# Kernel tuning notes

Hardware: AMD Instinct MI355X
Metric: run time of the kernel (lower is better)

The kernel has to match this reference:

```python
import jax, jax.numpy as jnp
import numpy as np

D_MODEL = 1024
NUM_HEADS = 16
HEAD_DIM = D_MODEL // NUM_HEADS          # 64
ROT_W = HEAD_DIM // 2                    # partial_factor=(0.0, 0.5) -> rotary on first half
MAX_LEN = 2048
BASE = 10000.0


def _rope_tables(max_len):
    # theta over even dims of ROT_W, each repeated twice (interleaved pairs): [t0,t0,t1,t1,...]
    theta = 1.0 / (BASE ** (np.arange(0, ROT_W, 2, dtype=np.float32) / ROT_W))  # [ROT_W/2]
    m = np.arange(max_len, dtype=np.float32)[:, None] * theta[None, :]          # [max_len, ROT_W/2]
    m = np.repeat(m, 2, axis=-1)                                                # [max_len, ROT_W]
    return jnp.asarray(np.cos(m)), jnp.asarray(np.sin(m))


def _rotate(x):
    # interleaved pairs (x0, x1) -> (-x1, x0)
    xr = x.reshape(x.shape[:-1] + (-1, 2))
    rot = jnp.stack([-xr[..., 1], xr[..., 0]], axis=-1)
    return rot.reshape(x.shape)


def setup_inputs() -> dict:
    key = jax.random.key(0)
    k1, k2, k3, k4 = jax.random.split(key, 4)
    B, L, H, E = 2, 2048, NUM_HEADS, HEAD_DIM
    return {
        "queries": jax.random.normal(k1, (B, L, H, E), jnp.float32),
        "keys": jax.random.normal(k2, (B, L, H, E), jnp.float32),
        "values": jax.random.normal(k3, (B, L, H, E), jnp.float32),
        "bias_weight": jax.random.normal(k4, (2, H), jnp.float32) * 0.02,  # BinaryAttentionBias embedding
        "n_vars": 32,
        "n_tokens": 64,
    }


def reference(queries, keys, values, bias_weight, n_vars, n_tokens):
    B, L, H, E = queries.shape
    q = queries.transpose(0, 2, 1, 3)  # [B,H,L,E]
    k = keys.transpose(0, 2, 1, 3)     # [B,H,L,E]

    # --- partial rotary projection (shared for q and k), seq_id = arange(L) ---
    cos, sin = _rope_tables(MAX_LEN)
    seq = jnp.arange(n_vars * n_tokens)
    c = cos[seq][None, None]  # [1,1,L,ROT_W]
    s = sin[seq][None, None]

    def rope(x):
        xr = x[..., :ROT_W]
        return jnp.concatenate([c * xr + s * _rotate(xr), x[..., ROT_W:]], axis=-1)

    q = rope(q)
    k = rope(k)

    scale = 1.0 / np.sqrt(E).astype(np.float32)

    # --- binary attention bias: per-head scalar by variable-id equality ---
    var_id = jnp.repeat(jnp.arange(n_vars), n_tokens)          # [L]
    same_var = var_id[:, None] == var_id[None, :]              # [L,L]
    bias = jnp.where(same_var[None, :, :],
                     bias_weight[1][:, None, None],
                     bias_weight[0][:, None, None])            # [H,L,L]

    # --- TimerMultivariateMask: causal in time, full across variables ---
    time_id = seq % n_tokens
    causal_bad = time_id[None, :] > time_id[:, None]           # key time > query time
    attn_mask = jnp.where(causal_bad[None], -jnp.inf, bias)    # [H,L,L]

    scores = jnp.einsum('bhle,bhse->bhls', q, k)               # [B,H,L,L]
    A = jax.nn.softmax(scale * scores + attn_mask[None], axis=-1)
    V = jnp.einsum('bhls,bshd->blhd', A, values)               # [B,L,H,E]
    return V
```

## Files before the change

kernel.cpp:

```cpp
#include <hip/hip_runtime.h>

typedef unsigned short u16;
typedef unsigned int u32;

typedef __attribute__((ext_vector_type(8))) __bf16 bf16x8;
typedef __attribute__((ext_vector_type(4))) float floatx4;

#define B_ 2
#define L_ 2048
#define H_ 16
#define E_ 64
#define QK_ELEMS (B_ * H_ * L_ * E_)
#define WS_OFF 128

static __device__ __forceinline__ float bf2f(u16 v) {
  u32 u = ((u32)v) << 16;
  return __builtin_bit_cast(float, u);
}
static __device__ __forceinline__ u16 f2bf(float x) {
  u32 u = __builtin_bit_cast(u32, x);
  u32 r = (u + 0x7FFFu + ((u >> 16) & 1u)) >> 16;
  return (u16)r;
}

static __device__ __forceinline__ u32 cvtpk_bf16(float lo, float hi) {
  u32 r;
  asm("v_cvt_pk_bf16_f32 %0, %1, %2" : "=v"(r) : "v"(lo), "v"(hi));
  return r;
}

static __device__ __forceinline__ float exp2_fast(float x) {
  float r;
  asm("v_exp_f32 %0, %1" : "=v"(r) : "v"(x));
  return r;
}

static __device__ __forceinline__ void sincos_fast(float a, float* s, float* c) {
  const float INV2PI = 0.15915494309189535f;
  float r = a * INV2PI;
  r = r - floorf(r);
  float ss, cc;
  asm("v_sin_f32 %0, %1" : "=v"(ss) : "v"(r));
  asm("v_cos_f32 %0, %1" : "=v"(cc) : "v"(r));
  *s = ss;
  *c = cc;
}

static __device__ __forceinline__ bool detect_f32_wave(const void* q) {
  u32 w = ((const u32*)q)[threadIdx.x & 63];
  int big = ((((w >> 7) & 0xFF) > 180) | (((w >> 23) & 0xFF) > 180));
  return __ballot(big) != 0ULL;
}

__global__ void detect_dtype(const u16* __restrict__ q, int* __restrict__ flag) {
  int lane = threadIdx.x;
  int big = 0;
#pragma unroll
  for (int i = 0; i < 16; ++i) {
    u16 v = q[lane * 16 + i];
    int e = (v >> 7) & 0xFF;
    big |= (e > 180);
  }
  unsigned long long b = __ballot(big);
  if (lane == 0) *flag = (b != 0ULL) ? 1 : 0;
}

static __device__ __forceinline__ bf16x8 ld8(const void* base, size_t off, bool f32) {
  if (f32) {
    const float* p = (const float*)base + off;
    float4 a = *(const float4*)p;
    float4 bb = *(const float4*)(p + 4);
    uint4 o;
    o.x = (u32)f2bf(a.x) | ((u32)f2bf(a.y) << 16);
    o.y = (u32)f2bf(a.z) | ((u32)f2bf(a.w) << 16);
    o.z = (u32)f2bf(bb.x) | ((u32)f2bf(bb.y) << 16);
    o.w = (u32)f2bf(bb.z) | ((u32)f2bf(bb.w) << 16);
    return __builtin_bit_cast(bf16x8, o);
  }
  return *(const bf16x8*)((const u16*)base + off);
}

static __device__ __forceinline__ bf16x8 rope_frag(bf16x8 x, float pos, int quad) {
  uint4 u = __builtin_bit_cast(uint4, x);
  float v0 = bf2f((u16)u.x), v1 = bf2f((u16)(u.x >> 16));
  float v2 = bf2f((u16)u.y), v3 = bf2f((u16)(u.y >> 16));
  float v4 = bf2f((u16)u.z), v5 = bf2f((u16)(u.z >> 16));
  float v6 = bf2f((u16)u.w), v7 = bf2f((u16)(u.w >> 16));
  const float LB = 0.83048202372184058696f;
  float jb = (float)(quad * 4);
  float a0 = pos * exp2_fast(-jb * LB);
  float a1 = pos * exp2_fast(-(jb + 1.f) * LB);
  float a2 = pos * exp2_fast(-(jb + 2.f) * LB);
  float a3 = pos * exp2_fast(-(jb + 3.f) * LB);
  float s0, c0, s1, c1, s2, c2, s3, c3;
  sincos_fast(a0, &s0, &c0);
  sincos_fast(a1, &s1, &c1);
  sincos_fast(a2, &s2, &c2);
  sincos_fast(a3, &s3, &c3);
  uint4 o;
  o.x = (u32)f2bf(c0 * v0 - s0 * v1) | ((u32)f2bf(c0 * v1 + s0 * v0) << 16);
  o.y = (u32)f2bf(c1 * v2 - s1 * v3) | ((u32)f2bf(c1 * v3 + s1 * v2) << 16);
  o.z = (u32)f2bf(c2 * v4 - s2 * v5) | ((u32)f2bf(c2 * v5 + s2 * v4) << 16);
  o.w = (u32)f2bf(c3 * v6 - s3 * v7) | ((u32)f2bf(c3 * v7 + s3 * v6) << 16);
  return __builtin_bit_cast(bf16x8, o);
}

__global__ __launch_bounds__(256) void prep_kv(
    const void* __restrict__ Q, const void* __restrict__ K, const void* __restrict__ V,
    u16* __restrict__ Kr, u16* __restrict__ VT) {
  __shared__ u16 tile[64][65];
  const int t = threadIdx.x;
  const bool f32 = detect_f32_wave(Q);

  if (blockIdx.x < (B_ * L_)) {
    const int bl = blockIdx.x;
    const int b = bl >> 11, l = bl & (L_ - 1);
    const int h = t >> 4, d = (t & 15) << 2;
    size_t in_off = (((size_t)(b * L_ + l) * H_ + h) * E_) + d;
    size_t out_off = (((size_t)(b * H_ + h) * L_ + l) * E_) + d;
    float k0, k1, k2, k3;
    if (f32) {
      float4 kv = *(const float4*)((const float*)K + in_off);
      k0 = kv.x; k1 = kv.y; k2 = kv.z; k3 = kv.w;
    } else {
      uint2 kv = *(const uint2*)((const u16*)K + in_off);
      k0 = bf2f((u16)kv.x); k1 = bf2f((u16)(kv.x >> 16));
      k2 = bf2f((u16)kv.y); k3 = bf2f((u16)(kv.y >> 16));
    }
    if (d < 32) {
      int j0 = d >> 1;
      const float LB = 0.83048202372184058696f;
      float a0 = (float)l * exp2_fast(-(float)j0 * LB);
      float a1 = (float)l * exp2_fast(-(float)(j0 + 1) * LB);
      float s0, c0, s1, c1;
      sincos_fast(a0, &s0, &c0);
      sincos_fast(a1, &s1, &c1);
      float r;
      r = c0 * k0 - s0 * k1; k1 = c0 * k1 + s0 * k0; k0 = r;
      r = c1 * k2 - s1 * k3; k3 = c1 * k3 + s1 * k2; k2 = r;
    }
    uint2 ko;
    ko.x = (u32)f2bf(k0) | ((u32)f2bf(k1) << 16);
    ko.y = (u32)f2bf(k2) | ((u32)f2bf(k3) << 16);
    *(uint2*)(Kr + out_off) = ko;
  } else {
    const int blk = blockIdx.x - (B_ * L_);
    const int bh = blk & 31, lt = blk >> 5;
    const int b = bh >> 4, h = bh & 15;
    const int l0 = lt << 6;
#pragma unroll
    for (int it = 0; it < 2; ++it) {
      int ll = (t >> 3) + (it << 5);
      int dc = (t & 7) << 3;
      size_t off = (((size_t)(b * L_ + l0 + ll) * H_ + h) * E_) + dc;
      bf16x8 x8 = ld8(V, off, f32);
      uint4 x = __builtin_bit_cast(uint4, x8);
      tile[ll][dc + 0] = (u16)x.x; tile[ll][dc + 1] = (u16)(x.x >> 16);
      tile[ll][dc + 2] = (u16)x.y; tile[ll][dc + 3] = (u16)(x.y >> 16);
      tile[ll][dc + 4] = (u16)x.z; tile[ll][dc + 5] = (u16)(x.z >> 16);
      tile[ll][dc + 6] = (u16)x.w; tile[ll][dc + 7] = (u16)(x.w >> 16);
    }
    __syncthreads();
    int e = t >> 2, lg = (t & 3) << 4;
    u32 pk[8];
#pragma unroll
    for (int i = 0; i < 8; ++i)
      pk[i] = (u32)tile[lg + 2 * i][e] | ((u32)tile[lg + 2 * i + 1][e] << 16);
    u16* dst = VT + (((size_t)(bh * 32 + lt)) << 12) + e * 64 + lg;
    uint4 o0; o0.x = pk[0]; o0.y = pk[1]; o0.z = pk[2]; o0.w = pk[3];
    uint4 o1; o1.x = pk[4]; o1.y = pk[5]; o1.z = pk[6]; o1.w = pk[7];
    *(uint4*)dst = o0;
    *(uint4*)(dst + 8) = o1;
  }
}

#if __has_builtin(__builtin_amdgcn_global_load_lds)
#define HAS_GLL 1
static __device__ __forceinline__ void gll16(const void* g, void* l) {
  __builtin_amdgcn_global_load_lds(
      (const __attribute__((address_space(1))) u32*)g,
      (__attribute__((address_space(3))) u32*)l, 16, 0, 0);
}
#else
#define HAS_GLL 0
#endif

__global__ __launch_bounds__(256, 2) void flash_v5(
    const void* __restrict__ Q, const u16* __restrict__ Kr,
    const u16* __restrict__ VT, const void* __restrict__ bw,
    void* __restrict__ out) {
  __shared__ u16 vbuf[2][64][64];
  __shared__ u32 plds[4][2][48][20];

  const int tid = threadIdx.x;
  const int wid = tid >> 6, lane = tid & 63;
  const int quad = lane >> 4, l16 = lane & 15;
  const int bh = blockIdx.x & 31;
  const int gb = blockIdx.x >> 5;
  const int var_l = (gb << 1) + (wid >> 1);
  const int s0 = (wid & 1) << 4;
  const int base = var_l << 6;
  const int b = bh >> 4, h = bh & 15;

  const bool f32 = detect_f32_wave(Q);
  const u16* Kb = Kr + ((size_t)bh << 17);
  const u16* Vb = VT + ((size_t)bh << 17);

  const float LOG2E = 1.4426950408889634f;
  const float bw_diff = f32 ? ((const float*)bw)[h] : bf2f(((const u16*)bw)[h]);
  const float bw_same = f32 ? ((const float*)bw)[H_ + h] : bf2f(((const u16*)bw)[H_ + h]);
  const float C1 = 0.125f * LOG2E;
  const float c2d = bw_diff * LOG2E;
  const float c2s = bw_same * LOG2E;
  const float NEGINF = -__builtin_inff();

  bf16x8 qf[2][2];
#pragma unroll
  for (int rh = 0; rh < 2; ++rh) {
    const int r = base + s0 + (rh << 5) + l16;
    size_t ro = (((size_t)(b * L_ + r) * H_ + h) * E_);
    qf[rh][0] = rope_frag(ld8(Q, ro + quad * 8, f32), (float)r, quad);
    qf[rh][1] = ld8(Q, ro + 32 + quad * 8, f32);
  }

  const floatx4 zero4 = {0.f, 0.f, 0.f, 0.f};
  bf16x8 ones;
  { uint4 t4; t4.x = t4.y = t4.z = t4.w = 0x3F803F80u; ones = __builtin_bit_cast(bf16x8, t4); }

  floatx4 oacc[2][4], lacc[2];
#pragma unroll
  for (int rh = 0; rh < 2; ++rh) {
    lacc[rh] = zero4;
#pragma unroll
    for (int c4 = 0; c4 < 4; ++c4) oacc[rh][c4] = zero4;
  }

  const int srow = lane >> 3;
  const int sc16 = (lane & 7) ^ srow;
  auto stage_issue = [&](int bufn, int v) {
#pragma unroll
    for (int rr = 0; rr < 2; ++rr) {
      const int chunk = (wid << 1) + rr;
      const u16* gv = Vb + ((size_t)v << 12) + (size_t)((chunk << 3) + srow) * 64 + sc16 * 8;
#if HAS_GLL
      gll16(gv, (char*)&vbuf[bufn][0][0] + chunk * 1024);
#else
      uint4 x = *(const uint4*)gv;
      *(uint4*)((u16*)&vbuf[bufn][0][0] + chunk * 512 + lane * 8) = x;
#endif
    }
  };

  stage_issue(0, 0);
  __asm__ volatile("s_waitcnt vmcnt(0)" ::: "memory");
  __syncthreads();

  int pp = 0;
  const int sw = l16 & 7;

  for (int v = 0; v < 32; ++v) {
    const int buf = v & 1;
    const int k0 = v << 6;

    bf16x8 kf[2][2], kg[2][2];
#pragma unroll
    for (int ch = 0; ch < 2; ++ch) {
      const u16* kr0 = Kb + (size_t)(k0 + ch * 16 + l16) * 64 + quad * 8;
      kf[ch][0] = *(const bf16x8*)kr0;
      kf[ch][1] = *(const bf16x8*)(kr0 + 32);
      const u16* kr1 = kr0 + 32 * 64;
      kg[ch][0] = *(const bf16x8*)kr1;
      kg[ch][1] = *(const bf16x8*)(kr1 + 32);
    }
    if (v < 31) stage_issue(buf ^ 1, v + 1);
    bf16x8 vf0[4], vf1[4];
#pragma unroll
    for (int c4 = 0; c4 < 4; ++c4) {
      vf0[c4] = *(const bf16x8*)&vbuf[buf][c4 * 16 + l16][(quad ^ sw) << 3];
      vf1[c4] = *(const bf16x8*)&vbuf[buf][c4 * 16 + l16][((4 + quad) ^ sw) << 3];
    }
    const float c2 = (v == var_l) ? c2s : c2d;

    floatx4 cc[2][2], dd[2];
#pragma unroll
    for (int ch = 0; ch < 2; ++ch) {
#pragma unroll
      for (int rh = 0; rh < 2; ++rh) {
        floatx4 a0 = __builtin_amdgcn_mfma_f32_16x16x32_bf16(kf[ch][0], qf[rh][0], zero4, 0, 0, 0);
        cc[rh][ch] = __builtin_amdgcn_mfma_f32_16x16x32_bf16(kf[ch][1], qf[rh][1], a0, 0, 0, 0);
      }
      floatx4 a1 = __builtin_amdgcn_mfma_f32_16x16x32_bf16(kg[ch][0], qf[1][0], zero4, 0, 0, 0);
      dd[ch] = __builtin_amdgcn_mfma_f32_16x16x32_bf16(kg[ch][1], qf[1][1], a1, 0, 0, 0);
    }

    u32* const prow = &plds[wid][pp][0][0];
#pragma unroll
    for (int ch = 0; ch < 2; ++ch) {
      float p0[4], p1[4], p2[4];
#pragma unroll
      for (int reg = 0; reg < 4; ++reg) {
        const bool msk = (ch * 16 + quad * 4 + reg) > (s0 + l16);
        float sA = fmaf(cc[0][ch][reg], C1, c2);
        if (msk) sA = NEGINF;
        p0[reg] = exp2_fast(sA);
        p1[reg] = exp2_fast(fmaf(cc[1][ch][reg], C1, c2));
        float sC = fmaf(dd[ch][reg], C1, c2);
        if (msk) sC = NEGINF;
        p2[reg] = exp2_fast(sC);
      }
      u32* w0 = prow + (0 + l16) * 20 + ch * 8 + quad * 2;
      w0[0] = cvtpk_bf16(p0[0], p0[1]);
      w0[1] = cvtpk_bf16(p0[2], p0[3]);
      u32* w1 = prow + (16 + l16) * 20 + ch * 8 + quad * 2;
      w1[0] = cvtpk_bf16(p1[0], p1[1]);
      w1[1] = cvtpk_bf16(p1[2], p1[3]);
      u32* w2 = prow + (32 + l16) * 20 + ch * 8 + quad * 2;
      w2[0] = cvtpk_bf16(p2[0], p2[1]);
      w2[1] = cvtpk_bf16(p2[2], p2[3]);
    }
    __asm__ volatile("s_waitcnt lgkmcnt(0)" ::: "memory");
    bf16x8 pa0, pa1, pb2;
    {
      const u32* r0 = prow + (0 + l16) * 20 + quad * 4;
      uint4 t4; t4.x = r0[0]; t4.y = r0[1]; t4.z = r0[2]; t4.w = r0[3];
      pa0 = __builtin_bit_cast(bf16x8, t4);
      const u32* r1 = prow + (16 + l16) * 20 + quad * 4;
      uint4 t5; t5.x = r1[0]; t5.y = r1[1]; t5.z = r1[2]; t5.w = r1[3];
      pa1 = __builtin_bit_cast(bf16x8, t5);
      const u32* r2 = prow + (32 + l16) * 20 + quad * 4;
      uint4 t6; t6.x = r2[0]; t6.y = r2[1]; t6.z = r2[2]; t6.w = r2[3];
      pb2 = __builtin_bit_cast(bf16x8, t6);
    }
    lacc[0] = __builtin_amdgcn_mfma_f32_16x16x32_bf16(pa0, ones, lacc[0], 0, 0, 0);
    lacc[1] = __builtin_amdgcn_mfma_f32_16x16x32_bf16(pa1, ones, lacc[1], 0, 0, 0);
    lacc[1] = __builtin_amdgcn_mfma_f32_16x16x32_bf16(pb2, ones, lacc[1], 0, 0, 0);
#pragma unroll
    for (int c4 = 0; c4 < 4; ++c4) {
      oacc[0][c4] = __builtin_amdgcn_mfma_f32_16x16x32_bf16(pa0, vf0[c4], oacc[0][c4], 0, 0, 0);
      oacc[1][c4] = __builtin_amdgcn_mfma_f32_16x16x32_bf16(pa1, vf0[c4], oacc[1][c4], 0, 0, 0);
      oacc[1][c4] = __builtin_amdgcn_mfma_f32_16x16x32_bf16(pb2, vf1[c4], oacc[1][c4], 0, 0, 0);
    }
    pp ^= 1;
    if (v < 31) {
      __asm__ volatile("s_waitcnt vmcnt(0)" ::: "memory");
      __syncthreads();
    }
  }

  float rinv[2][4];
#pragma unroll
  for (int rh = 0; rh < 2; ++rh)
#pragma unroll
    for (int reg = 0; reg < 4; ++reg) {
      float lv = lacc[rh][reg];
      rinv[rh][reg] = (lv > 1e-30f) ? 1.0f / lv : 0.0f;
    }

#pragma unroll
  for (int rh = 0; rh < 2; ++rh)
#pragma unroll
    for (int c4 = 0; c4 < 4; ++c4)
#pragma unroll
      for (int reg = 0; reg < 4; ++reg) {
        const int row = base + s0 + (rh << 5) + quad * 4 + reg;
        const int col = c4 * 16 + l16;
        float val = oacc[rh][c4][reg] * rinv[rh][reg];
        size_t oo = (((size_t)(b * L_ + row)) * H_ + h) * E_ + col;
        if (f32) ((float*)out)[oo] = val;
        else ((u16*)out)[oo] = f2bf(val);
      }
}

__global__ __launch_bounds__(256) void flash_fused(
    const void* __restrict__ Q, const void* __restrict__ K,
    const void* __restrict__ V, const void* __restrict__ bw,
    const int* __restrict__ flag, void* __restrict__ out) {
  __shared__ u16 plds[4][2][32 * 36];
  __shared__ u16 vlds[4][64][40];
  const bool f32 = flag ? (*flag != 0) : true;
  const int tid = threadIdx.x;
  const int wid = tid >> 6, lane = tid & 63;
  const int quad = lane >> 4, l16 = lane & 15;
  const int bh = blockIdx.x & 31;
  const int g = blockIdx.x >> 5;
  const int rowblk = (g << 2) + wid;
  const int row0 = rowblk << 5;
  const int b = bh >> 4, h = bh & 15;
  const int t0 = row0 & 63;
  const int var_l = row0 >> 6;
  const int ktiles = (t0 >> 5) + 1;

  const float bw_diff = f32 ? ((const float*)bw)[h] : bf2f(((const u16*)bw)[h]);
  const float bw_same = f32 ? ((const float*)bw)[H_ + h] : bf2f(((const u16*)bw)[H_ + h]);

  const floatx4 zero4 = {0.f, 0.f, 0.f, 0.f};
  bf16x8 ones;
  { uint4 t4; t4.x = t4.y = t4.z = t4.w = 0x3F803F80u; ones = __builtin_bit_cast(bf16x8, t4); }

  bf16x8 qf[2][2];
#pragma unroll
  for (int rh = 0; rh < 2; ++rh) {
    const int r = row0 + rh * 16 + l16;
    size_t ro = (((size_t)(b * L_ + r) * H_ + h) * E_);
#pragma unroll
    for (int hf = 0; hf < 2; ++hf)
      qf[rh][hf] = ld8(Q, ro + hf * 32 + quad * 8, f32);
    qf[rh][0] = rope_frag(qf[rh][0], (float)r, quad);
  }

  floatx4 oacc[2][4], lacc[2];
#pragma unroll
  for (int rh = 0; rh < 2; ++rh) {
    lacc[rh] = zero4;
#pragma unroll
    for (int c4 = 0; c4 < 4; ++c4) oacc[rh][c4] = zero4;
  }

  u16* const pbase = &plds[wid][0][0];
  u16* const vb = &vlds[wid][0][0];
  int pp = 0;

  for (int v = 0; v < 32; ++v) {
    const float bias = (v == var_l) ? bw_same : bw_diff;
    for (int kt = 0; kt < ktiles; ++kt) {
      const int k0 = (v << 6) + (kt << 5);

      bf16x8 kf[2][2];
#pragma unroll
      for (int ch = 0; ch < 2; ++ch) {
        const int r = k0 + ch * 16 + l16;
        size_t ro = (((size_t)(b * L_ + r) * H_ + h) * E_);
#pragma unroll
        for (int hf = 0; hf < 2; ++hf)
          kf[ch][hf] = ld8(K, ro + hf * 32 + quad * 8, f32);
        kf[ch][0] = rope_frag(kf[ch][0], (float)r, quad);
      }

      floatx4 cc[2][2];
#pragma unroll
      for (int rh = 0; rh < 2; ++rh)
#pragma unroll
        for (int ch = 0; ch < 2; ++ch) {
          floatx4 acc = __builtin_amdgcn_mfma_f32_16x16x32_bf16(qf[rh][0], kf[ch][0], zero4, 0, 0, 0);
          cc[rh][ch] = __builtin_amdgcn_mfma_f32_16x16x32_bf16(qf[rh][1], kf[ch][1], acc, 0, 0, 0);
        }

      u16* const pw = pbase + pp * (32 * 36);
      const int ts_b = (kt << 5) + l16;
#pragma unroll
      for (int rh = 0; rh < 2; ++rh)
#pragma unroll
        for (int ch = 0; ch < 2; ++ch) {
          const int ts = ts_b + ch * 16;
#pragma unroll
          for (int reg = 0; reg < 4; ++reg) {
            const int tl = t0 + rh * 16 + quad * 4 + reg;
            float s = cc[rh][ch][reg] * 0.125f + bias;
            float p = (ts > tl) ? 0.0f : __expf(s);
            pw[(rh * 16 + quad * 4 + reg) * 36 + ch * 16 + l16] = f2bf(p);
          }
        }

#pragma unroll
      for (int it = 0; it < 4; ++it) {
        const int s = (lane >> 3) + it * 8;
        const int dc = (lane & 7) << 3;
        size_t vo = (((size_t)(b * L_ + k0 + s) * H_ + h) * E_) + dc;
        bf16x8 x8 = ld8(V, vo, f32);
        uint4 x = __builtin_bit_cast(uint4, x8);
        vb[(dc + 0) * 40 + s] = (u16)x.x; vb[(dc + 1) * 40 + s] = (u16)(x.x >> 16);
        vb[(dc + 2) * 40 + s] = (u16)x.y; vb[(dc + 3) * 40 + s] = (u16)(x.y >> 16);
        vb[(dc + 4) * 40 + s] = (u16)x.z; vb[(dc + 5) * 40 + s] = (u16)(x.z >> 16);
        vb[(dc + 6) * 40 + s] = (u16)x.w; vb[(dc + 7) * 40 + s] = (u16)(x.w >> 16);
      }

      __asm__ volatile("s_waitcnt lgkmcnt(0)" ::: "memory");

      bf16x8 pa[2];
#pragma unroll
      for (int rh = 0; rh < 2; ++rh) {
        const u16* pr = pw + (rh * 16 + l16) * 36 + quad * 8;
        uint2 lo = *(const uint2*)pr;
        uint2 hi = *(const uint2*)(pr + 4);
        uint4 cmb; cmb.x = lo.x; cmb.y = lo.y; cmb.z = hi.x; cmb.w = hi.y;
        pa[rh] = __builtin_bit_cast(bf16x8, cmb);
      }

#pragma unroll
      for (int rh = 0; rh < 2; ++rh)
        lacc[rh] = __builtin_amdgcn_mfma_f32_16x16x32_bf16(pa[rh], ones, lacc[rh], 0, 0, 0);

#pragma unroll
      for (int c4 = 0; c4 < 4; ++c4) {
        bf16x8 vf = *(const bf16x8*)(vb + (c4 * 16 + l16) * 40 + quad * 8);
#pragma unroll
        for (int rh = 0; rh < 2; ++rh)
          oacc[rh][c4] = __builtin_amdgcn_mfma_f32_16x16x32_bf16(pa[rh], vf, oacc[rh][c4], 0, 0, 0);
      }
      pp ^= 1;
    }
  }

  float rinv[2][4];
#pragma unroll
  for (int rh = 0; rh < 2; ++rh)
#pragma unroll
    for (int reg = 0; reg < 4; ++reg) {
      float lv = lacc[rh][reg];
      rinv[rh][reg] = (lv > 1e-30f) ? 1.0f / lv : 0.0f;
    }

#pragma unroll
  for (int rh = 0; rh < 2; ++rh)
#pragma unroll
    for (int c4 = 0; c4 < 4; ++c4)
#pragma unroll
      for (int reg = 0; reg < 4; ++reg) {
        const int row = row0 + rh * 16 + quad * 4 + reg;
        const int col = c4 * 16 + l16;
        float val = oacc[rh][c4][reg] * rinv[rh][reg];
        size_t oo = (((size_t)(b * L_ + row)) * H_ + h) * E_ + col;
        if (f32) ((float*)out)[oo] = val;
        else ((u16*)out)[oo] = f2bf(val);
      }
}

extern "C" void kernel_launch(void* const* d_in, const int* in_sizes, int n_in,
                              void* d_out, int out_size, void* d_ws, size_t ws_size,
                              hipStream_t stream) {
  (void)in_sizes; (void)n_in; (void)out_size;
  const void* q = d_in[0];
  const void* k = d_in[1];
  const void* v = d_in[2];
  const void* bwp = d_in[3];
  const size_t need = (size_t)WS_OFF * 2 + 2u * QK_ELEMS * sizeof(u16);
  if (ws_size >= need) {
    u16* Kr = (u16*)d_ws + WS_OFF;
    u16* VT = Kr + QK_ELEMS;
    prep_kv<<<B_ * L_ + B_ * H_ * (L_ / 64), 256, 0, stream>>>(q, k, v, Kr, VT);
    flash_v5<<<512, 256, 0, stream>>>(q, Kr, VT, bwp, d_out);
  } else if (ws_size >= sizeof(int)) {
    int* flag = (int*)d_ws;
    detect_dtype<<<1, 64, 0, stream>>>((const u16*)q, flag);
    flash_fused<<<512, 256, 0, stream>>>(q, k, v, bwp, flag, d_out);
  } else {
    flash_fused<<<512, 256, 0, stream>>>(q, k, v, bwp, (const int*)nullptr, d_out);
  }
}
```

Measured before the change: 168.0 us.

## Stage K tiles through double-buffered LDS and raise MFMA wave priority

K fragments were previously read straight from global memory in each iteration. They are now prefetched, alongside V, into a double-buffered swizzled LDS tile using global_load_lds, and the prefetch is issued at the top of the loop. The change also wraps the MFMA sections in s_setprio, vectorizes the P writes and reads through LDS, and makes the dtype detection sample spread-out words from Q. This doubles the LDS staging footprint, which may affect occupancy, and the fallback path without global_load_lds now holds the staged data in registers.

```diff
diff --git a/kernel.cpp b/kernel.cpp
--- a/kernel.cpp
+++ b/kernel.cpp
@@ -46,9 +46,13 @@
   *c = cc;
 }
 
-static __device__ __forceinline__ bool detect_f32_wave(const void* q) {
-  u32 w = ((const u32*)q)[threadIdx.x & 63];
-  int big = ((((w >> 7) & 0xFF) > 180) | (((w >> 23) & 0xFF) > 180));
+static __device__ __forceinline__ bool detect_f32_spread(const void* q, u32 blk) {
+  const u32* q32 = (const u32*)q;
+  u32 off = ((blk & 1023u) << 6) + (threadIdx.x & 63);
+  u32 w0 = q32[off];
+  u32 w1 = q32[off + 65536];
+  int big = ((((w0 >> 7) & 0xFF) > 180) | (((w0 >> 23) & 0xFF) > 180) |
+             (((w1 >> 7) & 0xFF) > 180) | (((w1 >> 23) & 0xFF) > 180));
   return __ballot(big) != 0ULL;
 }
 
@@ -110,7 +114,7 @@
     u16* __restrict__ Kr, u16* __restrict__ VT) {
   __shared__ u16 tile[64][65];
   const int t = threadIdx.x;
-  const bool f32 = detect_f32_wave(Q);
+  const bool f32 = detect_f32_spread(Q, blockIdx.x);
 
   if (blockIdx.x < (B_ * L_)) {
     const int bl = blockIdx.x;
@@ -185,10 +189,11 @@
 #define HAS_GLL 0
 #endif
 
-__global__ __launch_bounds__(256, 2) void flash_v5(
+__global__ __launch_bounds__(256, 2) void flash_v6(
     const void* __restrict__ Q, const u16* __restrict__ Kr,
     const u16* __restrict__ VT, const void* __restrict__ bw,
     void* __restrict__ out) {
+  __shared__ u16 kbuf[2][64][64];
   __shared__ u16 vbuf[2][64][64];
   __shared__ u32 plds[4][2][48][20];
 
@@ -202,7 +207,7 @@
   const int base = var_l << 6;
   const int b = bh >> 4, h = bh & 15;
 
-  const bool f32 = detect_f32_wave(Q);
+  const bool f32 = detect_f32_spread(Q, blockIdx.x);
   const u16* Kb = Kr + ((size_t)bh << 17);
   const u16* Vb = VT + ((size_t)bh << 17);
 
@@ -237,21 +242,41 @@
 
   const int srow = lane >> 3;
   const int sc16 = (lane & 7) ^ srow;
+#if !HAS_GLL
+  uint4 sk[2], sv[2];
+#endif
   auto stage_issue = [&](int bufn, int v) {
+    const int k0r = v << 6;
 #pragma unroll
     for (int rr = 0; rr < 2; ++rr) {
       const int chunk = (wid << 1) + rr;
-      const u16* gv = Vb + ((size_t)v << 12) + (size_t)((chunk << 3) + srow) * 64 + sc16 * 8;
+      const int row = (chunk << 3) + srow;
+      const u16* gk = Kb + (size_t)(k0r + row) * 64 + sc16 * 8;
+      const u16* gv = Vb + ((size_t)v << 12) + (size_t)row * 64 + sc16 * 8;
 #if HAS_GLL
+      gll16(gk, (char*)&kbuf[bufn][0][0] + chunk * 1024);
       gll16(gv, (char*)&vbuf[bufn][0][0] + chunk * 1024);
 #else
-      uint4 x = *(const uint4*)gv;
-      *(uint4*)((u16*)&vbuf[bufn][0][0] + chunk * 512 + lane * 8) = x;
+      sk[rr] = *(const uint4*)gk;
+      sv[rr] = *(const uint4*)gv;
 #endif
     }
   };
+  auto stage_commit = [&](int bufn) {
+#if !HAS_GLL
+#pragma unroll
+    for (int rr = 0; rr < 2; ++rr) {
+      const int chunk = (wid << 1) + rr;
+      *(uint4*)((u16*)&kbuf[bufn][0][0] + chunk * 512 + lane * 8) = sk[rr];
+      *(uint4*)((u16*)&vbuf[bufn][0][0] + chunk * 512 + lane * 8) = sv[rr];
+    }
+#else
+    (void)bufn;
+#endif
+  };
 
   stage_issue(0, 0);
+  stage_commit(0);
   __asm__ volatile("s_waitcnt vmcnt(0)" ::: "memory");
   __syncthreads();
 
@@ -260,19 +285,19 @@
 
   for (int v = 0; v < 32; ++v) {
     const int buf = v & 1;
-    const int k0 = v << 6;
+    const bool more = (v < 31);
+    if (more) stage_issue(buf ^ 1, v + 1);
 
     bf16x8 kf[2][2], kg[2][2];
 #pragma unroll
     for (int ch = 0; ch < 2; ++ch) {
-      const u16* kr0 = Kb + (size_t)(k0 + ch * 16 + l16) * 64 + quad * 8;
-      kf[ch][0] = *(const bf16x8*)kr0;
-      kf[ch][1] = *(const bf16x8*)(kr0 + 32);
-      const u16* kr1 = kr0 + 32 * 64;
-      kg[ch][0] = *(const bf16x8*)kr1;
-      kg[ch][1] = *(const bf16x8*)(kr1 + 32);
-    }
-    if (v < 31) stage_issue(buf ^ 1, v + 1);
+      const int row = ch * 16 + l16;
+#pragma unroll
+      for (int hf = 0; hf < 2; ++hf) {
+        kf[ch][hf] = *(const bf16x8*)&kbuf[buf][row][(((hf << 2) + quad) ^ sw) << 3];
+        kg[ch][hf] = *(const bf16x8*)&kbuf[buf][32 + row][(((hf << 2) + quad) ^ sw) << 3];
+      }
+    }
     bf16x8 vf0[4], vf1[4];
 #pragma unroll
     for (int c4 = 0; c4 < 4; ++c4) {
@@ -282,6 +307,7 @@
     const float c2 = (v == var_l) ? c2s : c2d;
 
     floatx4 cc[2][2], dd[2];
+    __builtin_amdgcn_s_setprio(1);
 #pragma unroll
     for (int ch = 0; ch < 2; ++ch) {
 #pragma unroll
@@ -292,6 +318,7 @@
       floatx4 a1 = __builtin_amdgcn_mfma_f32_16x16x32_bf16(kg[ch][0], qf[1][0], zero4, 0, 0, 0);
       dd[ch] = __builtin_amdgcn_mfma_f32_16x16x32_bf16(kg[ch][1], qf[1][1], a1, 0, 0, 0);
     }
+    __builtin_amdgcn_s_setprio(0);
 
     u32* const prow = &plds[wid][pp][0][0];
 #pragma unroll
@@ -308,29 +335,21 @@
         if (msk) sC = NEGINF;
         p2[reg] = exp2_fast(sC);
       }
-      u32* w0 = prow + (0 + l16) * 20 + ch * 8 + quad * 2;
-      w0[0] = cvtpk_bf16(p0[0], p0[1]);
-      w0[1] = cvtpk_bf16(p0[2], p0[3]);
-      u32* w1 = prow + (16 + l16) * 20 + ch * 8 + quad * 2;
-      w1[0] = cvtpk_bf16(p1[0], p1[1]);
-      w1[1] = cvtpk_bf16(p1[2], p1[3]);
-      u32* w2 = prow + (32 + l16) * 20 + ch * 8 + quad * 2;
-      w2[0] = cvtpk_bf16(p2[0], p2[1]);
-      w2[1] = cvtpk_bf16(p2[2], p2[3]);
+      uint2 w;
+      w.x = cvtpk_bf16(p0[0], p0[1]); w.y = cvtpk_bf16(p0[2], p0[3]);
+      *(uint2*)(prow + (0 + l16) * 20 + ch * 8 + quad * 2) = w;
+      w.x = cvtpk_bf16(p1[0], p1[1]); w.y = cvtpk_bf16(p1[2], p1[3]);
+      *(uint2*)(prow + (16 + l16) * 20 + ch * 8 + quad * 2) = w;
+      w.x = cvtpk_bf16(p2[0], p2[1]); w.y = cvtpk_bf16(p2[2], p2[3]);
+      *(uint2*)(prow + (32 + l16) * 20 + ch * 8 + quad * 2) = w;
     }
     __asm__ volatile("s_waitcnt lgkmcnt(0)" ::: "memory");
     bf16x8 pa0, pa1, pb2;
-    {
-      const u32* r0 = prow + (0 + l16) * 20 + quad * 4;
-      uint4 t4; t4.x = r0[0]; t4.y = r0[1]; t4.z = r0[2]; t4.w = r0[3];
-      pa0 = __builtin_bit_cast(bf16x8, t4);
-      const u32* r1 = prow + (16 + l16) * 20 + quad * 4;
-      uint4 t5; t5.x = r1[0]; t5.y = r1[1]; t5.z = r1[2]; t5.w = r1[3];
-      pa1 = __builtin_bit_cast(bf16x8, t5);
-      const u32* r2 = prow + (32 + l16) * 20 + quad * 4;
-      uint4 t6; t6.x = r2[0]; t6.y = r2[1]; t6.z = r2[2]; t6.w = r2[3];
-      pb2 = __builtin_bit_cast(bf16x8, t6);
-    }
+    pa0 = __builtin_bit_cast(bf16x8, *(const uint4*)(prow + (0 + l16) * 20 + quad * 4));
+    pa1 = __builtin_bit_cast(bf16x8, *(const uint4*)(prow + (16 + l16) * 20 + quad * 4));
+    pb2 = __builtin_bit_cast(bf16x8, *(const uint4*)(prow + (32 + l16) * 20 + quad * 4));
+
+    __builtin_amdgcn_s_setprio(1);
     lacc[0] = __builtin_amdgcn_mfma_f32_16x16x32_bf16(pa0, ones, lacc[0], 0, 0, 0);
     lacc[1] = __builtin_amdgcn_mfma_f32_16x16x32_bf16(pa1, ones, lacc[1], 0, 0, 0);
     lacc[1] = __builtin_amdgcn_mfma_f32_16x16x32_bf16(pb2, ones, lacc[1], 0, 0, 0);
@@ -340,8 +359,11 @@
       oacc[1][c4] = __builtin_amdgcn_mfma_f32_16x16x32_bf16(pa1, vf0[c4], oacc[1][c4], 0, 0, 0);
       oacc[1][c4] = __builtin_amdgcn_mfma_f32_16x16x32_bf16(pb2, vf1[c4], oacc[1][c4], 0, 0, 0);
     }
+    __builtin_amdgcn_s_setprio(0);
     pp ^= 1;
-    if (v < 31) {
+
+    if (more) {
+      stage_commit(buf ^ 1);
       __asm__ volatile("s_waitcnt vmcnt(0)" ::: "memory");
       __syncthreads();
     }
@@ -538,7 +560,7 @@
     u16* Kr = (u16*)d_ws + WS_OFF;
     u16* VT = Kr + QK_ELEMS;
     prep_kv<<<B_ * L_ + B_ * H_ * (L_ / 64), 256, 0, stream>>>(q, k, v, Kr, VT);
-    flash_v5<<<512, 256, 0, stream>>>(q, Kr, VT, bwp, d_out);
+    flash_v6<<<512, 256, 0, stream>>>(q, Kr, VT, bwp, d_out);
   } else if (ws_size >= sizeof(int)) {
     int* flag = (int*)d_ws;
     detect_dtype<<<1, 64, 0, stream>>>((const u16*)q, flag);
```

Measured after the change: 144.7 us. -13.9%, faster.
